# Performance work log

Hardware: AMD Instinct MI355X
Metric: run time of the kernel (lower is better)

## Reference

```python
import jax, jax.numpy as jnp
import numpy as np

D, P, S, E = 200, 200, 150, 150  # drugs, proteins, diseases, side-effects
EMB = 256

def setup_inputs() -> dict:
    key = jax.random.key(0)
    ks = jax.random.split(key, 10)
    s = 0.05
    type_mask = jnp.concatenate([
        jnp.zeros(D, jnp.int64) if False else jnp.full((D,), 0, jnp.int32),
        jnp.full((P,), 1, jnp.int32),
        jnp.full((S,), 2, jnp.int32),
        jnp.full((E,), 3, jnp.int32)]).astype(jnp.int32)
    return {
        'type_mask': type_mask,
        'entity_embedding': jax.random.normal(ks[0], (D + P + S + E, EMB)) * s,
        'relation_embedding': jax.random.normal(ks[1], (1200, EMB)) * s,
        'W_ent': jax.random.normal(ks[2], (EMB, EMB)) * s,
        'W_rel': jax.random.normal(ks[3], (EMB, EMB)) * s,
        'W1': jax.random.normal(ks[4], (2 * EMB, 1024)) * s,
        'b1': jnp.zeros((1024,)),
        'W2': jax.random.normal(ks[5], (1024, 512)) * s,
        'b2': jnp.zeros((512,)),
        'W3': jax.random.normal(ks[6], (512, 2)) * s,
        'b3': jnp.zeros((2,)),
    }

def _pair_softmax(a, b, W1, b1, W2, b2, W3, b3):
    # classifier(concat(a[i], b[j])) for the full cartesian product.
    # First linear is decomposed: W1 @ [a;b] = a@W1a + b@W1b (same math,
    # avoids materializing the [Na*Nb, 2*EMB] concat tensor).
    W1a, W1b = W1[:EMB], W1[EMB:]
    ha = a @ W1a                      # [Na, 1024]
    hb = b @ W1b                      # [Nb, 1024]
    h = jax.nn.relu(ha[:, None, :] + hb[None, :, :] + b1)  # [Na, Nb, 1024]
    h = jax.nn.relu(h @ W2 + b2)      # [Na, Nb, 512]
    logits = h @ W3 + b3              # [Na, Nb, 2]
    Na, Nb = a.shape[0], b.shape[0]
    return jax.nn.softmax(logits.reshape(Na * Nb, 2), axis=-1)

def reference(type_mask, entity_embedding, relation_embedding, W_ent, W_rel,
              W1, b1, W2, b2, W3, b3):
    tm = np.asarray(type_mask)  # concrete, block-structured type ids
    idx = [np.nonzero(tm == t)[0] for t in range(4)]
    # project embeddings (project_on path; nn.Linear: x @ W)
    ent = entity_embedding @ W_ent
    _rel = relation_embedding @ W_rel  # computed in original forward, unused (graph_on off)
    drug, prot, dis, se = (ent[idx[0]], ent[idx[1]], ent[idx[2]], ent[idx[3]])
    cls = lambda a, b: _pair_softmax(a, b, W1, b1, W2, b2, W3, b3)
    out_dp = cls(drug, prot)
    out_dd = cls(drug, drug)
    out_ds = cls(drug, dis)
    out_de = cls(drug, se)
    out_ps = cls(prot, dis)
    out_pp = cls(prot, prot)
    out_pd = cls(prot, drug)
    out_ed = cls(se, drug)
    out_sp = cls(dis, prot)
    out_sd = cls(dis, drug)
    return (out_dp, out_dd, out_ds, out_de, out_ps, out_pp, out_pd,
            out_ed, out_sp, out_sd, drug)
```

## Files before the change

### kernel.cpp

```cpp
#include <hip/hip_runtime.h>
#include <hip/hip_bf16.h>

typedef __attribute__((ext_vector_type(4))) float floatx4;
typedef __attribute__((ext_vector_type(8))) __bf16 bf16x8;
typedef unsigned short ushort_t;

#define NENT  700
#define EMB   256
#define KDIM  1024
#define NDIM  512
#define HROWS 720
#define NPAIR 340000

#define WS_HA   0
#define WS_HB   (WS_HA + HROWS*KDIM*2)
#define WS_W2H  (WS_HB + HROWS*KDIM*2)
#define WS_ENT  (WS_W2H + NDIM*KDIM*2)
#define WS_LG   (WS_ENT + NENT*EMB*4)

__device__ __forceinline__ float ldin(const void* p, int i, int isbf) {
    return isbf ? __bfloat162float(((const __hip_bfloat16*)p)[i])
                : ((const float*)p)[i];
}

__device__ __forceinline__ int detect_bf16(const ushort_t* __restrict__ w) {
    int t = threadIdx.x & 63;
    int e = (w[2*t] >> 7) & 0xFF;
    unsigned long long m = __ballot(e >= 100 && e <= 126);
    return (__popcll(m) >= 48) ? 1 : 0;
}

#define LDS_BARRIER() do { __builtin_amdgcn_s_waitcnt(0xC07F); __builtin_amdgcn_s_barrier(); } while (0)

__global__ void prep_kernel(const void* __restrict__ E, const void* __restrict__ Went,
                            const void* __restrict__ W1, const void* __restrict__ b1,
                            const void* __restrict__ W2, __hip_bfloat16* __restrict__ W2H,
                            __hip_bfloat16* __restrict__ HA, __hip_bfloat16* __restrict__ HB,
                            void* __restrict__ out) {
    int isbf = detect_bf16((const ushort_t*)E);
    if (blockIdx.x < 90) {
        int part = blockIdx.x / 45;
        int ib = (blockIdx.x % 45) * 16;
        int t = threadIdx.x;
        __shared__ float eL[16][EMB];
        __shared__ float rows[16][EMB];
#pragma unroll
        for (int r = 0; r < 16; ++r) {
            int i = ib + r;
            eL[r][t] = (i < NENT) ? ldin(E, i*EMB + t, isbf) : 0.f;
        }
        __syncthreads();
        float a16[16];
#pragma unroll
        for (int r = 0; r < 16; ++r) a16[r] = 0.f;
        if (isbf) {
            const __hip_bfloat16* W = (const __hip_bfloat16*)Went;
            for (int k = 0; k < EMB; ++k) {
                float w = __bfloat162float(W[k*EMB + t]);
#pragma unroll
                for (int r = 0; r < 16; ++r) a16[r] += eL[r][k] * w;
            }
        } else {
            const float* W = (const float*)Went;
            for (int k = 0; k < EMB; ++k) {
                float w = W[k*EMB + t];
#pragma unroll
                for (int r = 0; r < 16; ++r) a16[r] += eL[r][k] * w;
            }
        }
#pragma unroll
        for (int r = 0; r < 16; ++r) {
            rows[r][t] = a16[r];
            int i = ib + r;
            if (!part && i < 200) {
                if (isbf) ((__hip_bfloat16*)out)[680000 + i*EMB + t] = __float2bfloat16(a16[r]);
                else      ((float*)out)[680000 + i*EMB + t] = a16[r];
            }
        }
        __syncthreads();

        float acc[16][4];
#pragma unroll
        for (int r = 0; r < 16; ++r)
#pragma unroll
            for (int p = 0; p < 4; ++p) acc[r][p] = 0.f;

        int wbase = part*EMB*KDIM;
        if (isbf) {
            const __hip_bfloat16* W = (const __hip_bfloat16*)W1;
            for (int k = 0; k < EMB; ++k) {
                float w[4];
#pragma unroll
                for (int p = 0; p < 4; ++p) w[p] = __bfloat162float(W[wbase + k*KDIM + t + p*256]);
#pragma unroll
                for (int r = 0; r < 16; ++r) {
                    float e = rows[r][k];
#pragma unroll
                    for (int p = 0; p < 4; ++p) acc[r][p] += e * w[p];
                }
            }
        } else {
            const float* W = (const float*)W1;
            for (int k = 0; k < EMB; ++k) {
                float w[4];
#pragma unroll
                for (int p = 0; p < 4; ++p) w[p] = W[wbase + k*KDIM + t + p*256];
#pragma unroll
                for (int r = 0; r < 16; ++r) {
                    float e = rows[r][k];
#pragma unroll
                    for (int p = 0; p < 4; ++p) acc[r][p] += e * w[p];
                }
            }
        }
        __hip_bfloat16* HX = part ? HB : HA;
#pragma unroll
        for (int r = 0; r < 16; ++r) {
#pragma unroll
            for (int p = 0; p < 4; ++p) {
                int n = t + p*256;
                float v = acc[r][p];
                if (!part) v += ldin(b1, n, isbf);
                HX[(ib + r)*KDIM + n] = __float2bfloat16(v);
            }
        }
    } else {
        int g = (blockIdx.x - 90)*256 + threadIdx.x;
        int lane = g & 63, f = (g >> 6) & 15, kc = (g >> 10) & 31, half = g >> 15;
        int l15 = lane & 15, quad = lane >> 4;
        int n = half*256 + f*16 + l15;
        bf16x8 v;
#pragma unroll
        for (int j = 0; j < 8; ++j) {
            int k = kc*32 + quad*8 + j;
            v[j] = (__bf16)ldin(W2, k*NDIM + n, isbf);
        }
        *(bf16x8*)(W2H + (size_t)g*8) = v;
    }
}

union U8 { bf16x8 v; unsigned u[4]; };

__device__ __forceinline__ bf16x8 mk_af3(bf16x8 ha, bf16x8 hb) {
    U8 r;
#pragma unroll
    for (int j = 0; j < 4; ++j) {
        float x0 = fmaxf((float)ha[2*j]   + (float)hb[2*j],   0.f);
        float x1 = fmaxf((float)ha[2*j+1] + (float)hb[2*j+1], 0.f);
        unsigned u0 = __float_as_uint(x0) + 0x8000u;
        unsigned u1 = __float_as_uint(x1) + 0x8000u;
#if defined(__has_builtin) && __has_builtin(__builtin_amdgcn_perm)
        r.u[j] = __builtin_amdgcn_perm(u1, u0, 0x07060302u);
#else
        r.u[j] = (u0 >> 16) | (u1 & 0xFFFF0000u);
#endif
    }
    return r.v;
}

#define MFMA(a, b, c) __builtin_amdgcn_mfma_f32_16x16x32_bf16((a), (b), (c), 0, 0, 0)

__global__ __launch_bounds__(256, 2) void pair_kernel(
        const ushort_t* __restrict__ HA, const ushort_t* __restrict__ HB,
        const ushort_t* __restrict__ W2H, const void* __restrict__ E,
        const void* __restrict__ b2, const void* __restrict__ W3,
        const void* __restrict__ b3, void* __restrict__ out) {

    const int blkEnd[10] = {650,1300,1800,2300,2800,3450,4100,4594,5088,5582};
    const int aB[10]  = {0,0,0,0,200,200,200,550,400,400};
    const int bB[10]  = {200,0,400,550,400,200,0,0,200,0};
    const int NaT[10] = {200,200,200,200,200,200,200,150,150,150};
    const int NbT[10] = {200,200,150,150,150,200,200,200,200,200};
    const int jTl[10] = {13,13,10,10,10,13,13,13,13,13};
    const int oOf[10] = {0,80000,160000,220000,280000,340000,420000,500000,560000,620000};

    __shared__ __align__(16) unsigned char sAF[16384];
    __shared__ float lgt[4][64][2];

    int bid = blockIdx.x;
    int ty = 0;
    while (bid >= blkEnd[ty]) ty++;
    int lb = bid - (ty ? blkEnd[ty-1] : 0);
    int jT = jTl[ty];
    int it = lb / jT;
    int jt = lb - it*jT;
    int i0 = aB[ty] + it*4;
    int j0 = bB[ty] + jt*16;

    int tid  = threadIdx.x;
    int lane = tid & 63;
    int w    = tid >> 6;
    int kcw  = w & 1;
    int mp   = (w >> 1) * 2;
    int l15  = lane & 15;
    int quad = lane >> 4;
    int kb   = (bid*7) & 31;

    const char* WB0 = (const char*)W2H + (size_t)(w*4)*1024 + lane*16;
    const char* WB1 = WB0 + (size_t)512*1024;
    const ushort_t* HBp  = HB + (j0 + l15)*KDIM + quad*8;
    const ushort_t* HAp0 = HA + (i0 + mp)*KDIM + quad*8;
    const ushort_t* HAp1 = HAp0 + KDIM;

    floatx4 acc[4][8];
#pragma unroll
    for (int mf = 0; mf < 4; ++mf)
#pragma unroll
        for (int hf = 0; hf < 8; ++hf) acc[mf][hf] = (floatx4){0.f,0.f,0.f,0.f};

    bf16x8 Bc[2][4], Bn[2][4];
    int k0 = kb, k1 = (kb + 1) & 31;
#pragma unroll
    for (int nf = 0; nf < 4; ++nf) {
        Bc[0][nf] = *(const bf16x8*)(WB0 + (size_t)k0*16384 + nf*1024);
        Bc[1][nf] = *(const bf16x8*)(WB1 + (size_t)k0*16384 + nf*1024);
        Bn[0][nf] = *(const bf16x8*)(WB0 + (size_t)k1*16384 + nf*1024);
        Bn[1][nf] = *(const bf16x8*)(WB1 + (size_t)k1*16384 + nf*1024);
    }
    int kg0 = (kb + kcw) & 31;
    bf16x8 ha0 = *(const bf16x8*)(HAp0 + kg0*32);
    bf16x8 ha1 = *(const bf16x8*)(HAp1 + kg0*32);
    bf16x8 hb  = *(const bf16x8*)(HBp + kg0*32);

#pragma unroll 1
    for (int ph = 0; ph < 16; ++ph) {
        char* sW = (char*)sAF + (ph & 1)*8192 + kcw*4096 + mp*1024 + lane*16;
        *(bf16x8*)(sW)        = mk_af3(ha0, hb);
        *(bf16x8*)(sW + 1024) = mk_af3(ha1, hb);
        int kgn = (kb + 2*ph + 2 + kcw) & 31;
        ha0 = *(const bf16x8*)(HAp0 + kgn*32);
        ha1 = *(const bf16x8*)(HAp1 + kgn*32);
        hb  = *(const bf16x8*)(HBp + kgn*32);
        LDS_BARRIER();

        const char* sR = (const char*)sAF + (ph & 1)*8192 + lane*16;
        int kn2 = (kb + 2*ph + 2) & 31;
        int kn3 = (kb + 2*ph + 3) & 31;
#pragma unroll
        for (int m = 0; m < 4; ++m) {
            bf16x8 a = *(const bf16x8*)(sR + m*1024);
#pragma unroll
            for (int hf = 0; hf < 8; ++hf)
                acc[m][hf] = MFMA(a, Bc[hf>>2][hf&3], acc[m][hf]);
        }
#pragma unroll
        for (int nf = 0; nf < 4; ++nf) {
            Bc[0][nf] = *(const bf16x8*)(WB0 + (size_t)kn2*16384 + nf*1024);
            Bc[1][nf] = *(const bf16x8*)(WB1 + (size_t)kn2*16384 + nf*1024);
        }
#pragma unroll
        for (int m = 0; m < 4; ++m) {
            bf16x8 a = *(const bf16x8*)(sR + 4096 + m*1024);
#pragma unroll
            for (int hf = 0; hf < 8; ++hf)
                acc[m][hf] = MFMA(a, Bn[hf>>2][hf&3], acc[m][hf]);
        }
#pragma unroll
        for (int nf = 0; nf < 4; ++nf) {
            Bn[0][nf] = *(const bf16x8*)(WB0 + (size_t)kn3*16384 + nf*1024);
            Bn[1][nf] = *(const bf16x8*)(WB1 + (size_t)kn3*16384 + nf*1024);
        }
    }

    int isbf = detect_bf16((const ushort_t*)E);
    float b2v[8], wa[8], wb[8];
#pragma unroll
    for (int hf = 0; hf < 8; ++hf) {
        int n = (hf >> 2)*256 + w*64 + (hf & 3)*16 + l15;
        b2v[hf] = ldin(b2, n, isbf);
        wa[hf]  = ldin(W3, 2*n, isbf);
        wb[hf]  = ldin(W3, 2*n+1, isbf);
    }
#pragma unroll
    for (int mf = 0; mf < 4; ++mf) {
        float s0[4] = {0.f,0.f,0.f,0.f};
        float s1[4] = {0.f,0.f,0.f,0.f};
#pragma unroll
        for (int hf = 0; hf < 8; ++hf) {
            floatx4 c = acc[mf][hf];
#pragma unroll
            for (int r = 0; r < 4; ++r) {
                float v = fmaxf(c[r] + b2v[hf], 0.f);
                s0[r] += v * wa[hf];
                s1[r] += v * wb[hf];
            }
        }
#pragma unroll
        for (int off = 1; off < 16; off <<= 1) {
#pragma unroll
            for (int r = 0; r < 4; ++r) {
                s0[r] += __shfl_xor(s0[r], off, 64);
                s1[r] += __shfl_xor(s1[r], off, 64);
            }
        }
        if (l15 == 0) {
#pragma unroll
            for (int r = 0; r < 4; ++r) {
                int p = mf*16 + quad*4 + r;
                lgt[w][p][0] = s0[r];
                lgt[w][p][1] = s1[r];
            }
        }
    }
    __syncthreads();

    if (tid < 64) {
        int p = tid;
        float l0 = lgt[0][p][0] + lgt[1][p][0] + lgt[2][p][0] + lgt[3][p][0];
        float l1 = lgt[0][p][1] + lgt[1][p][1] + lgt[2][p][1] + lgt[3][p][1];
        l0 += ldin(b3, 0, isbf);
        l1 += ldin(b3, 1, isbf);
        int pi = it*4 + (p >> 4), pj = jt*16 + (p & 15);
        if (pi < NaT[ty] && pj < NbT[ty]) {
            float mx = fmaxf(l0, l1);
            float e0 = __expf(l0 - mx), e1 = __expf(l1 - mx);
            float inv = 1.f / (e0 + e1);
            int o = oOf[ty] + (pi*NbT[ty] + pj)*2;
            if (isbf) {
                __hip_bfloat16* ob = (__hip_bfloat16*)out;
                ob[o]   = __float2bfloat16(e0 * inv);
                ob[o+1] = __float2bfloat16(e1 * inv);
            } else {
                float* of = (float*)out;
                of[o]   = e0 * inv;
                of[o+1] = e1 * inv;
            }
        }
    }
}

extern "C" void kernel_launch(void* const* d_in, const int* in_sizes, int n_in,
                              void* d_out, int out_size, void* d_ws, size_t ws_size,
                              hipStream_t stream) {
    const void* E    = d_in[1];
    const void* Went = d_in[3];
    const void* W1   = d_in[5];
    const void* b1   = d_in[6];
    const void* W2   = d_in[7];
    const void* b2   = d_in[8];
    const void* W3   = d_in[9];
    const void* b3   = d_in[10];

    char* ws = (char*)d_ws;
    __hip_bfloat16* HA   = (__hip_bfloat16*)(ws + WS_HA);
    __hip_bfloat16* HB   = (__hip_bfloat16*)(ws + WS_HB);
    __hip_bfloat16* W2H  = (__hip_bfloat16*)(ws + WS_W2H);

    prep_kernel<<<dim3(346), dim3(256), 0, stream>>>(E, Went, W1, b1, W2, W2H, HA, HB, d_out);
    pair_kernel<<<dim3(5582), dim3(256), 0, stream>>>((const ushort_t*)HA, (const ushort_t*)HB,
                                                      (const ushort_t*)W2H, E, b2, W3, b3, d_out);
}
```

Baseline: 489.2 us.

## Split prep projection across more blocks and raise MFMA wave priority

The prep kernel's entity/W1 projection is redistributed from 90 blocks of 16 rows x 1024 columns to 720 blocks of 8 rows x 256 columns, so more CUs share the small prep stage. The cost is that each block now recomputes the entity projection (E @ W_ent) for its rows, repeated across four column slices. The pair kernel also wraps its MFMA bursts in s_setprio(1) so these waves get issue priority over the interleaved global loads.

```diff
diff --git a/kernel.cpp b/kernel.cpp
--- a/kernel.cpp
+++ b/kernel.cpp
@@ -38,94 +38,79 @@
                             __hip_bfloat16* __restrict__ HA, __hip_bfloat16* __restrict__ HB,
                             void* __restrict__ out) {
     int isbf = detect_bf16((const ushort_t*)E);
-    if (blockIdx.x < 90) {
-        int part = blockIdx.x / 45;
-        int ib = (blockIdx.x % 45) * 16;
-        int t = threadIdx.x;
-        __shared__ float eL[16][EMB];
-        __shared__ float rows[16][EMB];
-#pragma unroll
-        for (int r = 0; r < 16; ++r) {
+    if (blockIdx.x < 720) {
+        int part = blockIdx.x & 1;
+        int ns   = (blockIdx.x >> 1) & 3;
+        int rt   = blockIdx.x >> 3;
+        int ib   = rt * 8;
+        int t    = threadIdx.x;
+        __shared__ float eL[8][EMB];
+        __shared__ float rows[8][EMB];
+#pragma unroll
+        for (int r = 0; r < 8; ++r) {
             int i = ib + r;
             eL[r][t] = (i < NENT) ? ldin(E, i*EMB + t, isbf) : 0.f;
         }
         __syncthreads();
-        float a16[16];
-#pragma unroll
-        for (int r = 0; r < 16; ++r) a16[r] = 0.f;
+        float a8[8];
+#pragma unroll
+        for (int r = 0; r < 8; ++r) a8[r] = 0.f;
         if (isbf) {
             const __hip_bfloat16* W = (const __hip_bfloat16*)Went;
             for (int k = 0; k < EMB; ++k) {
                 float w = __bfloat162float(W[k*EMB + t]);
 #pragma unroll
-                for (int r = 0; r < 16; ++r) a16[r] += eL[r][k] * w;
+                for (int r = 0; r < 8; ++r) a8[r] += eL[r][k] * w;
             }
         } else {
             const float* W = (const float*)Went;
             for (int k = 0; k < EMB; ++k) {
                 float w = W[k*EMB + t];
 #pragma unroll
-                for (int r = 0; r < 16; ++r) a16[r] += eL[r][k] * w;
-            }
-        }
-#pragma unroll
-        for (int r = 0; r < 16; ++r) {
-            rows[r][t] = a16[r];
+                for (int r = 0; r < 8; ++r) a8[r] += eL[r][k] * w;
+            }
+        }
+#pragma unroll
+        for (int r = 0; r < 8; ++r) {
+            rows[r][t] = a8[r];
             int i = ib + r;
-            if (!part && i < 200) {
-                if (isbf) ((__hip_bfloat16*)out)[680000 + i*EMB + t] = __float2bfloat16(a16[r]);
-                else      ((float*)out)[680000 + i*EMB + t] = a16[r];
+            if (!part && !ns && i < 200) {
+                if (isbf) ((__hip_bfloat16*)out)[680000 + i*EMB + t] = __float2bfloat16(a8[r]);
+                else      ((float*)out)[680000 + i*EMB + t] = a8[r];
             }
         }
         __syncthreads();
 
-        float acc[16][4];
-#pragma unroll
-        for (int r = 0; r < 16; ++r)
-#pragma unroll
-            for (int p = 0; p < 4; ++p) acc[r][p] = 0.f;
-
+        int n = ns*256 + t;
+        float acc[8];
+#pragma unroll
+        for (int r = 0; r < 8; ++r) acc[r] = 0.f;
         int wbase = part*EMB*KDIM;
         if (isbf) {
             const __hip_bfloat16* W = (const __hip_bfloat16*)W1;
             for (int k = 0; k < EMB; ++k) {
-                float w[4];
-#pragma unroll
-                for (int p = 0; p < 4; ++p) w[p] = __bfloat162float(W[wbase + k*KDIM + t + p*256]);
-#pragma unroll
-                for (int r = 0; r < 16; ++r) {
-                    float e = rows[r][k];
-#pragma unroll
-                    for (int p = 0; p < 4; ++p) acc[r][p] += e * w[p];
-                }
+                float w = __bfloat162float(W[wbase + k*KDIM + n]);
+#pragma unroll
+                for (int r = 0; r < 8; ++r) acc[r] += rows[r][k] * w;
             }
         } else {
             const float* W = (const float*)W1;
             for (int k = 0; k < EMB; ++k) {
-                float w[4];
-#pragma unroll
-                for (int p = 0; p < 4; ++p) w[p] = W[wbase + k*KDIM + t + p*256];
-#pragma unroll
-                for (int r = 0; r < 16; ++r) {
-                    float e = rows[r][k];
-#pragma unroll
-                    for (int p = 0; p < 4; ++p) acc[r][p] += e * w[p];
-                }
+                float w = W[wbase + k*KDIM + n];
+#pragma unroll
+                for (int r = 0; r < 8; ++r) acc[r] += rows[r][k] * w;
             }
         }
         __hip_bfloat16* HX = part ? HB : HA;
-#pragma unroll
-        for (int r = 0; r < 16; ++r) {
-#pragma unroll
-            for (int p = 0; p < 4; ++p) {
-                int n = t + p*256;
-                float v = acc[r][p];
-                if (!part) v += ldin(b1, n, isbf);
-                HX[(ib + r)*KDIM + n] = __float2bfloat16(v);
-            }
+        float bv = part ? 0.f : ldin(b1, n, isbf);
+#pragma unroll
+        for (int r = 0; r < 8; ++r) {
+            float v = acc[r];
+            if (!part) v += bv;
+            HX[(ib + r)*KDIM + n] = __float2bfloat16(v);
         }
     } else {
-        int g = (blockIdx.x - 90)*256 + threadIdx.x;
+        int g = (blockIdx.x - 720)*256 + threadIdx.x;
         int lane = g & 63, f = (g >> 6) & 15, kc = (g >> 10) & 31, half = g >> 15;
         int l15 = lane & 15, quad = lane >> 4;
         int n = half*256 + f*16 + l15;
@@ -236,6 +221,7 @@
         const char* sR = (const char*)sAF + (ph & 1)*8192 + lane*16;
         int kn2 = (kb + 2*ph + 2) & 31;
         int kn3 = (kb + 2*ph + 3) & 31;
+        __builtin_amdgcn_s_setprio(1);
 #pragma unroll
         for (int m = 0; m < 4; ++m) {
             bf16x8 a = *(const bf16x8*)(sR + m*1024);
@@ -243,11 +229,13 @@
             for (int hf = 0; hf < 8; ++hf)
                 acc[m][hf] = MFMA(a, Bc[hf>>2][hf&3], acc[m][hf]);
         }
+        __builtin_amdgcn_s_setprio(0);
 #pragma unroll
         for (int nf = 0; nf < 4; ++nf) {
             Bc[0][nf] = *(const bf16x8*)(WB0 + (size_t)kn2*16384 + nf*1024);
             Bc[1][nf] = *(const bf16x8*)(WB1 + (size_t)kn2*16384 + nf*1024);
         }
+        __builtin_amdgcn_s_setprio(1);
 #pragma unroll
         for (int m = 0; m < 4; ++m) {
             bf16x8 a = *(const bf16x8*)(sR + 4096 + m*1024);
@@ -255,6 +243,7 @@
             for (int hf = 0; hf < 8; ++hf)
                 acc[m][hf] = MFMA(a, Bn[hf>>2][hf&3], acc[m][hf]);
         }
+        __builtin_amdgcn_s_setprio(0);
 #pragma unroll
         for (int nf = 0; nf < 4; ++nf) {
             Bn[0][nf] = *(const bf16x8*)(WB0 + (size_t)kn3*16384 + nf*1024);
@@ -346,7 +335,7 @@
     __hip_bfloat16* HB   = (__hip_bfloat16*)(ws + WS_HB);
     __hip_bfloat16* W2H  = (__hip_bfloat16*)(ws + WS_W2H);
 
-    prep_kernel<<<dim3(346), dim3(256), 0, stream>>>(E, Went, W1, b1, W2, W2H, HA, HB, d_out);
+    prep_kernel<<<dim3(976), dim3(256), 0, stream>>>(E, Went, W1, b1, W2, W2H, HA, HB, d_out);
     pair_kernel<<<dim3(5582), dim3(256), 0, stream>>>((const ushort_t*)HA, (const ushort_t*)HB,
                                                       (const ushort_t*)W2H, E, b2, W3, b3, d_out);
 }
```

After: 461.7 us. 1.06x faster.
